# Kernel optimization log

Hardware: AMD Instinct MI355X
Metric: run time of the kernel (lower is better)

The kernel has to match this reference:

```python
import jax, jax.numpy as jnp
import numpy as np

IMG = 128                  # img_size
FMM = 35.0
SENSOR = 32.0
FUV = FMM * IMG / SENSOR   # focal length in pixels (screen space, in_ndc=False)
N_PTS = 16384
CHUNK = 1024               # points per scan step
R_SIL = 0.008              # silhouette pass radius (NDC)
R_DEP = 0.012              # depth pass radius (NDC)
K_SIL = 8
K_DEP = 16
DIST = 1.2


def _look_at(dist, elev_deg, azim_deg):
    # PyTorch3D look_at_view_transform with at=origin, up=+Y, degrees=True
    elev = jnp.deg2rad(elev_deg)
    azim = jnp.deg2rad(azim_deg)
    cam = jnp.stack([dist * jnp.cos(elev) * jnp.sin(azim),
                     dist * jnp.sin(elev),
                     dist * jnp.cos(elev) * jnp.cos(azim)], axis=-1)  # (B,3)
    up = jnp.array([0.0, 1.0, 0.0], dtype=cam.dtype)
    z_ax = -cam / (jnp.linalg.norm(cam, axis=-1, keepdims=True) + 1e-8)
    x_ax = jnp.cross(jnp.broadcast_to(up, z_ax.shape), z_ax)
    x_ax = x_ax / (jnp.linalg.norm(x_ax, axis=-1, keepdims=True) + 1e-8)
    y_ax = jnp.cross(z_ax, x_ax)
    R = jnp.stack([x_ax, y_ax, z_ax], axis=-1)   # columns are camera axes
    T = -jnp.einsum('bi,bij->bj', cam, R)        # X_cam = X_world @ R + T
    return R, T


def _project(pts, R, T):
    # world -> camera (row-vector convention) -> screen px -> PyTorch3D NDC
    Xc = jnp.einsum('bni,bij->bnj', pts, R) + T[:, None, :]
    z = Xc[..., 2]
    z_safe = jnp.where(z > 1e-5, z, 1.0)  # points behind camera are culled anyway
    xs = FUV * Xc[..., 0] / z_safe + IMG / 2.0
    ys = FUV * Xc[..., 1] / z_safe + IMG / 2.0
    x_ndc = 1.0 - 2.0 * xs / IMG
    y_ndc = 1.0 - 2.0 * ys / IMG
    return jnp.stack([x_ndc, y_ndc], axis=-1), z


def _rasterize(xy, z, r2, K):
    """Per-pixel K nearest-in-depth points within per-point NDC radius.
    xy: (B,N,2) NDC, z: (B,N) camera depth, r2: (B,N) squared radius.
    Returns zbuf, dists of shape (B,IMG,IMG,K), -1 for empty slots."""
    B, N, _ = xy.shape
    P = IMG * IMG
    # pixel-center NDC grid (PyTorch3D: +X left, +Y up; row-major flatten)
    gxs = 1.0 - (2.0 * jnp.arange(IMG, dtype=xy.dtype) + 1.0) / IMG  # per column
    gys = 1.0 - (2.0 * jnp.arange(IMG, dtype=xy.dtype) + 1.0) / IMG  # per row
    gx = jnp.tile(gxs, IMG)          # (P,)
    gy = jnp.repeat(gys, IMG)        # (P,)

    nch = N // CHUNK
    px = xy[..., 0].reshape(B, nch, CHUNK).swapaxes(0, 1)
    py = xy[..., 1].reshape(B, nch, CHUNK).swapaxes(0, 1)
    pz = z.reshape(B, nch, CHUNK).swapaxes(0, 1)
    pr2 = r2.reshape(B, nch, CHUNK).swapaxes(0, 1)

    def body(carry, c):
        top_z, top_d = carry
        cx, cy, cz, cr2 = c                               # each (B,CHUNK)
        dx = gx[None, :, None] - cx[:, None, :]           # (B,P,CHUNK)
        dy = gy[None, :, None] - cy[:, None, :]
        d2 = dx * dx + dy * dy
        ok = (d2 < cr2[:, None, :]) & (cz[:, None, :] > 0.0)
        zc = jnp.where(ok, cz[:, None, :], jnp.inf)
        cand_z = jnp.concatenate([top_z, zc], axis=-1)    # (B,P,K+CHUNK)
        cand_d = jnp.concatenate([top_d, d2], axis=-1)
        negz, idx = jax.lax.top_k(-cand_z, K)             # K smallest depths
        return (-negz, jnp.take_along_axis(cand_d, idx, axis=-1)), None

    init = (jnp.full((B, P, K), jnp.inf, dtype=xy.dtype),
            jnp.zeros((B, P, K), dtype=xy.dtype))
    (top_z, top_d), _ = jax.lax.scan(jax.checkpoint(body), init, (px, py, pz, pr2))
    valid = jnp.isfinite(top_z)
    zbuf = jnp.where(valid, top_z, -1.0).reshape(B, IMG, IMG, K)
    dists = jnp.where(valid, top_d, -1.0).reshape(B, IMG, IMG, K)
    return zbuf, dists


def setup_inputs() -> dict:
    key = jax.random.key(0)
    k1, k2 = jax.random.split(key)
    point_cloud = jax.random.normal(k1, (2, N_PTS, 6), dtype=jnp.float32) * 0.25
    param = jax.random.normal(k2, (2, 8, 3), dtype=jnp.float32) * 20.0  # degrees
    return {"point_cloud": point_cloud, "param": param}


def reference(point_cloud, param):
    pts = point_cloud[..., :3]
    B = pts.shape[0]
    elev0 = param[:, 1, 0]
    azim0 = param[:, 0, 0]

    # ---- silhouette pass (radius 0.008, K=8) + alpha compositing ----
    R0, T0 = _look_at(DIST, elev0, azim0)
    xy0, z0 = _project(pts, R0, T0)
    r2_sil = jnp.full((B, N_PTS), R_SIL * R_SIL, dtype=pts.dtype)
    _, dists_s = _rasterize(xy0, z0, r2_sil, K_SIL)
    alphas = jnp.where(dists_s >= 0.0, 1.0 - dists_s / (R_SIL * R_SIL), 0.0)
    trans = jnp.cumprod(1.0 - alphas, axis=-1)
    trans_excl = jnp.concatenate([jnp.ones_like(trans[..., :1]), trans[..., :-1]], axis=-1)
    sihlt_map = jnp.sum(alphas * trans_excl, axis=-1, keepdims=True) * 255.0  # (B,H,W,1)

    # ---- depth pass with random view (radius 0.012, K=16) ----
    kd = jax.random.key(42)
    ke, ka = jax.random.split(kd)
    elev_d = jax.random.uniform(ke, (B,), dtype=pts.dtype) * 60.0 - 30.0
    azim_d = jax.random.uniform(ka, (B,), dtype=pts.dtype) * 300.0 + azim0 + 30.0
    Rd, Td = _look_at(DIST, elev_d, azim_d)
    xyd, zd = _project(pts, Rd, Td)
    r2_dep = jnp.full((B, N_PTS), R_DEP * R_DEP, dtype=pts.dtype)
    zbuf_d, _ = _rasterize(xyd, zd, r2_dep, K_DEP)
    depth_ini = zbuf_d[..., 0]

    # density-aware adaptive radius (detached, per source .detach())
    area = jnp.sum((jax.lax.stop_gradient(depth_ini) > 0.0).astype(pts.dtype), axis=(1, 2))
    pa_radius = area / 16384.0 * 0.057                      # (B,)
    r2_ada = jnp.broadcast_to((pa_radius * pa_radius)[:, None], (B, N_PTS))

    zbuf_a, dists_a = _rasterize(xyd, zd, r2_ada, K_DEP)
    depth_img = zbuf_a[..., :8]
    dist_top = dists_a[..., :8]
    return (sihlt_map, depth_img, dist_top)
```

## Files before the change

kernel.cpp:

```cpp
#include <hip/hip_runtime.h>
#include <hip/hip_cooperative_groups.h>
#include <cstring>
#include <cstdint>

namespace cg = cooperative_groups;

#define NPTS 16384
#define FUVC 140.0f
#define R_SILF 0.008f
#define R_DEPF 0.012f
#define R2_SIL (0.008f*0.008f)
#define R2_DEP (0.012f*0.012f)
#define CH 512

#define AREA_OFF  48
#define PA_OFF    50
#define R2ADA_OFF 52
#define TICK0     54
#define TICK1     55
#define CNT_SIL   64
#define OFF_SIL   2112
#define CNT_ADA   4160
#define OFF_ADA   6208
#define FLAGS8    8256
#define FLAGS     8256
#define ZERO_END  16448
#define PROJ0     41024
#define PROJ1     172096
#define LSILF     303168
#define LADAF     827456
#define WS1_WORDS 2007104u
#define WS1_NEEDED ((size_t)WS1_WORDS * 4u)
#define LSIL      303168
#define LADA      434240
#define WS2_WORDS 729152u
#define WS2_NEEDED ((size_t)WS2_WORDS * 4u)

#define FUSED_BLOCKS 1024
#define FUSED_NT (FUSED_BLOCKS * 256)

__device__ __forceinline__ void cam_calc(float elev, float azim, float c[12]) {
    const float D2R = 0.017453292519943295f;
    float er = elev * D2R, ar = azim * D2R;
    float ce = cosf(er), se = sinf(er), ca = cosf(ar), sa = sinf(ar);
    float cx = 1.2f * ce * sa, cy = 1.2f * se, cz = 1.2f * ce * ca;
    float n = sqrtf(cx*cx + cy*cy + cz*cz) + 1e-8f;
    float zx = -cx / n, zy = -cy / n, zz = -cz / n;
    float xx = zz, xy = 0.0f, xz = -zx;
    float xn = sqrtf(xx*xx + xy*xy + xz*xz) + 1e-8f;
    xx /= xn; xz /= xn;
    float yx = zy*xz - zz*xy, yy = zz*xx - zx*xz, yz = zx*xy - zy*xx;
    c[0]=xx; c[1]=xy; c[2]=xz; c[3]=yx; c[4]=yy; c[5]=yz;
    c[6]=zx; c[7]=zy; c[8]=zz;
    c[9]  = -(cx*xx + cy*xy + cz*xz);
    c[10] = -(cx*yx + cy*yy + cz*yz);
    c[11] = -(cx*zx + cy*zy + cz*zz);
}

__device__ __forceinline__ void cam_compute(const float* __restrict__ param,
                                            float* __restrict__ ws,
                                            int t, float ue0, float ue1,
                                            float ua0, float ua1) {
    int b = t >> 1, cam = t & 1;
    float azim0 = param[b * 24 + 0];
    float elev0 = param[b * 24 + 3];
    float elev, azim;
    if (cam == 0) { elev = elev0; azim = azim0; }
    else {
        float ue = b ? ue1 : ue0;
        float ua = b ? ua1 : ua0;
        elev = ue * 60.0f - 30.0f;
        azim = ua * 300.0f + azim0 + 30.0f;
    }
    float c[12];
    cam_calc(elev, azim, c);
    float* w = ws + t * 12;
    #pragma unroll
    for (int i = 0; i < 12; i++) w[i] = c[i];
}

__device__ __forceinline__ float4 project_pt(const float* __restrict__ P,
                                             const float c[12]) {
    float X = P[0], Y = P[1], Z = P[2];
    float xc = X*c[0] + Y*c[1] + Z*c[2] + c[9];
    float yc = X*c[3] + Y*c[4] + Z*c[5] + c[10];
    float zc = X*c[6] + Y*c[7] + Z*c[8] + c[11];
    float zs = zc > 1e-5f ? zc : 1.0f;
    float px = 1.0f - (FUVC * xc / zs + 64.0f) * (1.0f/64.0f);
    float py = 1.0f - (FUVC * yc / zs + 64.0f) * (1.0f/64.0f);
    return make_float4(px, py, zc, 0.0f);
}

__device__ __forceinline__ void pix_range(float p, float r, int& lo, int& hi) {
    float lo_f = (1.0f - p - r) * 64.0f - 0.5f;
    float hi_f = (1.0f - p + r) * 64.0f - 0.5f;
    lo = (int)ceilf(lo_f - 1e-3f);
    hi = (int)floorf(hi_f + 1e-3f);
    lo = max(lo, 0); hi = min(hi, 127);
}

__device__ __forceinline__ void bin_bbox(float4 q, float r, int& bxl, int& bxh,
                                         int& byl, int& byh) {
    bxl = 0; bxh = -1; byl = 0; byh = -1;
    if (q.z > 0.0f) {
        int cl, chh, rl, rh;
        pix_range(q.x, r, cl, chh);
        pix_range(q.y, r, rl, rh);
        if (cl <= chh && rl <= rh) {
            bxl = cl >> 2; bxh = chh >> 2; byl = rl >> 2; byh = rh >> 2;
        }
    }
}

__device__ __forceinline__ void top8_insert(float z, float d,
                                            float tz[8], float td[8]) {
    #pragma unroll
    for (int k = 0; k < 8; k++) {
        bool lt = z < tz[k];
        float oz = tz[k], od = td[k];
        if (lt) { tz[k] = z; td[k] = d; z = oz; d = od; }
    }
}

__device__ __forceinline__ void hit_test(float4 pt, float gx, float gy, float r2,
                                         float tz[8], float td[8]) {
    float dx = gx - pt.x, dy = gy - pt.y;
    float d2 = dx*dx + dy*dy;
    if (d2 < r2 && pt.z > 0.0f && pt.z < tz[7]) top8_insert(pt.z, d2, tz, td);
}

#define CE8(i, j) { bool sw = mz[j] < mz[i]; \
    float t1 = mz[i], t2 = md[i]; \
    mz[i] = sw ? mz[j] : mz[i]; md[i] = sw ? md[j] : md[i]; \
    mz[j] = sw ? t1 : mz[j];    md[j] = sw ? t2 : md[j]; }

__device__ __forceinline__ void merge_sorted8(float tz[8], float td[8], int mask) {
    float oz[8], od[8];
    #pragma unroll
    for (int k = 0; k < 8; k++) {
        oz[k] = __shfl_xor(tz[k], mask);
        od[k] = __shfl_xor(td[k], mask);
    }
    float mz[8], md[8];
    #pragma unroll
    for (int k = 0; k < 8; k++) {
        bool take = oz[7 - k] < tz[k];
        mz[k] = take ? oz[7 - k] : tz[k];
        md[k] = take ? od[7 - k] : td[k];
    }
    CE8(0,4) CE8(1,5) CE8(2,6) CE8(3,7)
    CE8(0,2) CE8(1,3) CE8(4,6) CE8(5,7)
    CE8(0,1) CE8(2,3) CE8(4,5) CE8(6,7)
    #pragma unroll
    for (int k = 0; k < 8; k++) { tz[k] = mz[k]; td[k] = md[k]; }
}

__device__ __forceinline__ void merge_seq8(float tz[8], float td[8],
                                           const float* __restrict__ ozp,
                                           const float* __restrict__ odp) {
    float mz[8], md[8];
    #pragma unroll
    for (int k = 0; k < 8; k++) {
        float oz = ozp[7 - k], od = odp[7 - k];
        bool take = oz < tz[k];
        mz[k] = take ? oz : tz[k];
        md[k] = take ? od : td[k];
    }
    CE8(0,4) CE8(1,5) CE8(2,6) CE8(3,7)
    CE8(0,2) CE8(1,3) CE8(4,6) CE8(5,7)
    CE8(0,1) CE8(2,3) CE8(4,5) CE8(6,7)
    #pragma unroll
    for (int k = 0; k < 8; k++) { tz[k] = mz[k]; td[k] = md[k]; }
}

__device__ __forceinline__ void scan1024(unsigned* uw, unsigned cbase,
                                         unsigned obase, unsigned* s, int t) {
    unsigned c0 = uw[cbase + t*4 + 0];
    unsigned c1 = uw[cbase + t*4 + 1];
    unsigned c2 = uw[cbase + t*4 + 2];
    unsigned c3 = uw[cbase + t*4 + 3];
    unsigned tot = c0 + c1 + c2 + c3;
    s[t] = tot; __syncthreads();
    for (int off = 1; off < 256; off <<= 1) {
        unsigned v = (t >= off) ? s[t - off] : 0u;
        __syncthreads();
        s[t] += v;
        __syncthreads();
    }
    unsigned base = s[t] - tot;
    uw[obase + t*4 + 0] = base;
    uw[obase + t*4 + 1] = base + c0;
    uw[obase + t*4 + 2] = base + c0 + c1;
    uw[obase + t*4 + 3] = base + c0 + c1 + c2;
    uw[cbase + t*4 + 0] = 0;
    uw[cbase + t*4 + 1] = 0;
    uw[cbase + t*4 + 2] = 0;
    uw[cbase + t*4 + 3] = 0;
}

__device__ __forceinline__ void body_area_scan(float* __restrict__ ws, int job,
                                               int t, unsigned* s) {
    unsigned* uw = (unsigned*)ws;
    if (job < 2) {
        int b = job;
        unsigned acc = 0;
        #pragma unroll
        for (int j = 0; j < 16; j++) {
            unsigned w = uw[FLAGS8 + b * 4096 + t * 16 + j];
            acc += __popc(w & 0x01010101u);
        }
        s[t] = acc; __syncthreads();
        for (int off = 128; off > 0; off >>= 1) {
            if (t < off) s[t] += s[t + off];
            __syncthreads();
        }
        if (t == 0) {
            unsigned area = s[0];
            uw[AREA_OFF + b] = area;
            float pa = (float)area * (1.0f/16384.0f) * 0.057f;
            ws[PA_OFF + b] = pa;
            ws[R2ADA_OFF + b] = pa * pa;
        }
    } else {
        int b = job - 2;
        scan1024(uw, CNT_SIL + b * 1024, OFF_SIL + b * 1024, s, t);
    }
}

__device__ __forceinline__ void body_cnt_ada(float* __restrict__ ws, int p) {
    unsigned* uw = (unsigned*)ws;
    int b = p >> 14;
    float4 q = ((const float4*)(ws + PROJ1))[p];
    float pa = ws[PA_OFF + b];
    int bxl, bxh, byl, byh;
    bin_bbox(q, pa, bxl, bxh, byl, byh);
    for (int by = byl; by <= byh; by++)
        for (int bx = bxl; bx <= bxh; bx++)
            atomicAdd(&uw[CNT_ADA + b * 1024 + by * 32 + bx], 1u);
}

__device__ __forceinline__ void body_scat_sil(float* __restrict__ ws, int p) {
    unsigned* uw = (unsigned*)ws;
    int b = p >> 14;
    float4 q = ((const float4*)(ws + PROJ0))[p];
    int bxl, bxh, byl, byh;
    bin_bbox(q, R_SILF, bxl, bxh, byl, byh);
    for (int by = byl; by <= byh; by++)
        for (int bx = bxl; bx <= bxh; bx++) {
            unsigned bin = b * 1024 + by * 32 + bx;
            unsigned idx = uw[OFF_SIL + bin] + atomicAdd(&uw[CNT_SIL + bin], 1u);
            ((float4*)(ws + LSILF))[b * 65536 + idx] = q;
        }
}

__device__ __forceinline__ void body_scan_ada(float* __restrict__ ws, int b, int t) {
    unsigned* uw = (unsigned*)ws;
    unsigned c[16]; unsigned tot = 0;
    #pragma unroll
    for (int j = 0; j < 16; j++) { c[j] = uw[CNT_ADA + b * 1024 + t * 16 + j]; tot += c[j]; }
    unsigned inc = tot;
    #pragma unroll
    for (int off = 1; off < 64; off <<= 1) {
        unsigned v = __shfl_up(inc, off);
        if (t >= off) inc += v;
    }
    unsigned base = inc - tot;
    #pragma unroll
    for (int j = 0; j < 16; j++) {
        uw[OFF_ADA + b * 1024 + t * 16 + j] = base;
        base += c[j];
        uw[CNT_ADA + b * 1024 + t * 16 + j] = 0u;
    }
}

__device__ __forceinline__ void body_scat_ada(float* __restrict__ ws, int p) {
    unsigned* uw = (unsigned*)ws;
    int b = p >> 14;
    float4 q = ((const float4*)(ws + PROJ1))[p];
    float pa = ws[PA_OFF + b];
    int bxl, bxh, byl, byh;
    bin_bbox(q, pa, bxl, bxh, byl, byh);
    for (int by = byl; by <= byh; by++)
        for (int bx = bxl; bx <= bxh; bx++) {
            unsigned bin = b * 1024 + by * 32 + bx;
            unsigned idx = uw[OFF_ADA + bin] + atomicAdd(&uw[CNT_ADA + bin], 1u);
            ((float4*)(ws + LADAF))[b * 147456 + idx] = q;
        }
}

__device__ __forceinline__ void body_gather256(const float* __restrict__ ws,
                                               float* __restrict__ out,
                                               int id, int t,
                                               float* __restrict__ sm) {
    const unsigned* uw = (const unsigned*)ws;
    bool sil = id < 2048;
    int gt = sil ? id : id - 2048;
    int b = gt >> 10;
    int tile = gt & 1023;
    int p = t & 15, seg = t >> 4;
    int bx = tile & 31, by = tile >> 5;
    int col = (bx << 2) + (p & 3), row = (by << 2) + (p >> 2);
    float gx = 1.0f - (float)(2*col + 1) * (1.0f/128.0f);
    float gy = 1.0f - (float)(2*row + 1) * (1.0f/128.0f);
    float r2 = sil ? R2_SIL : ws[R2ADA_OFF + b];
    unsigned start = sil ? uw[OFF_SIL + b * 1024 + tile] : uw[OFF_ADA + b * 1024 + tile];
    unsigned len   = sil ? uw[CNT_SIL + b * 1024 + tile] : uw[CNT_ADA + b * 1024 + tile];
    const float4* lst = sil ? ((const float4*)(ws + LSILF)) + b * 65536 + start
                            : ((const float4*)(ws + LADAF)) + b * 147456 + start;

    float tz[8], td[8];
    #pragma unroll
    for (int k = 0; k < 8; k++) { tz[k] = INFINITY; td[k] = 0.0f; }

    unsigned i = (unsigned)seg;
    while (i + 112 < len) {
        float4 cb[8];
        #pragma unroll
        for (int u = 0; u < 8; u++) cb[u] = lst[i + 16u * (unsigned)u];
        #pragma unroll
        for (int u = 0; u < 8; u++) hit_test(cb[u], gx, gy, r2, tz, td);
        i += 128;
    }
    for (; i < len; i += 16) hit_test(lst[i], gx, gy, r2, tz, td);

    merge_sorted8(tz, td, 16);
    merge_sorted8(tz, td, 32);

    int w = t >> 6;
    if ((t & 63) < 16) {
        float* dst = sm + (w * 16 + p) * 17;
        #pragma unroll
        for (int k = 0; k < 8; k++) { dst[k] = tz[k]; dst[8 + k] = td[k]; }
    }
    __syncthreads();
    if (t < 16) {
        #pragma unroll
        for (int ww = 1; ww < 4; ww++) {
            const float* src = sm + (ww * 16 + p) * 17;
            merge_seq8(tz, td, src, src + 8);
        }
        int pix = (b << 14) + row * 128 + col;
        if (sil) {
            float trans = 1.0f, acc = 0.0f;
            #pragma unroll
            for (int k = 0; k < 8; k++) {
                float a = (tz[k] != INFINITY) ? (1.0f - td[k] / R2_SIL) : 0.0f;
                acc += a * trans;
                trans *= (1.0f - a);
            }
            out[pix] = acc * 255.0f;
        } else {
            float* dep = out + 32768  + (size_t)pix * 8;
            float* dst = out + 294912 + (size_t)pix * 8;
            #pragma unroll
            for (int k = 0; k < 8; k++) {
                bool v = (tz[k] != INFINITY);
                dep[k] = v ? tz[k] : -1.0f;
                dst[k] = v ? td[k] : -1.0f;
            }
        }
    }
}

__global__ __launch_bounds__(256) void k_fusedp(const float* __restrict__ pc,
                                                const float* __restrict__ param,
                                                float* __restrict__ ws,
                                                float* __restrict__ out,
                                                float ue0, float ue1,
                                                float ua0, float ua1) {
    cg::grid_group grid = cg::this_grid();
    unsigned* uw = (unsigned*)ws;
    __shared__ unsigned sh[2048];
    __shared__ unsigned shLast;
    int t = threadIdx.x;
    int tid = blockIdx.x * 256 + t;

    for (int i = 48 + tid; i < ZERO_END; i += FUSED_NT) uw[i] = 0u;
    if (tid < 4) cam_compute(param, ws, tid, ue0, ue1, ua0, ua1);
    grid.sync();

    if (blockIdx.x < 128) {
        int b = blockIdx.x >> 6;
        int p = ((blockIdx.x & 63) << 8) + t;
        unsigned char* fb = (unsigned char*)(uw + FLAGS8);
        const float* P = pc + ((size_t)b * NPTS + p) * 6;
        float c0[12], c1[12];
        const float* w0 = ws + (b * 2) * 12;
        #pragma unroll
        for (int i = 0; i < 12; i++) { c0[i] = w0[i]; c1[i] = w0[12 + i]; }

        #pragma unroll
        for (int j = 0; j < 4; j++) sh[t * 4 + j] = 0u;
        __syncthreads();

        float4 q0 = project_pt(P, c0);
        ((float4*)(ws + PROJ0))[b * NPTS + p] = q0;
        int bxl, bxh, byl, byh;
        bin_bbox(q0, R_SILF, bxl, bxh, byl, byh);
        for (int by = byl; by <= byh; by++)
            for (int bx = bxl; bx <= bxh; bx++)
                atomicAdd(&sh[by * 32 + bx], 1u);

        float4 q1 = project_pt(P, c1);
        ((float4*)(ws + PROJ1))[b * NPTS + p] = q1;
        if (q1.z > 0.0f) {
            int cl, chh, rl, rh;
            pix_range(q1.x, R_DEPF, cl, chh);
            pix_range(q1.y, R_DEPF, rl, rh);
            for (int rr = rl; rr <= rh; rr++) {
                float gyv = 1.0f - (float)(2 * rr + 1) * (1.0f/128.0f);
                float dy = gyv - q1.y;
                for (int cc = cl; cc <= chh; cc++) {
                    float gxv = 1.0f - (float)(2 * cc + 1) * (1.0f/128.0f);
                    float dx = gxv - q1.x;
                    if (dx*dx + dy*dy < R2_DEP) fb[b * NPTS + rr * 128 + cc] = 1;
                }
            }
        }
        __syncthreads();
        #pragma unroll
        for (int j = 0; j < 4; j++) {
            unsigned c = sh[t * 4 + j];
            if (c) atomicAdd(&uw[CNT_SIL + b * 1024 + t * 4 + j], c);
        }
        __threadfence();
    }
    if (t == 0) shLast = (atomicAdd(&uw[TICK0], 1u) == FUSED_BLOCKS - 1) ? 1u : 0u;
    __syncthreads();
    if (shLast) {
        __threadfence();
        for (int job = 0; job < 4; job++) {
            body_area_scan(ws, job, t, sh);
            __syncthreads();
        }
        __threadfence();
    }
    grid.sync();

    if (blockIdx.x < 128) {
        int b = blockIdx.x >> 6;
        int p = ((blockIdx.x & 63) << 8) + t;
        float4 q = ((const float4*)(ws + PROJ1))[b * NPTS + p];
        float pa = ws[PA_OFF + b];
        #pragma unroll
        for (int j = 0; j < 4; j++) sh[t * 4 + j] = 0u;
        __syncthreads();
        int bxl, bxh, byl, byh;
        bin_bbox(q, pa, bxl, bxh, byl, byh);
        for (int by = byl; by <= byh; by++)
            for (int bx = bxl; bx <= bxh; bx++)
                atomicAdd(&sh[by * 32 + bx], 1u);
        __syncthreads();
        #pragma unroll
        for (int j = 0; j < 4; j++) {
            unsigned c = sh[t * 4 + j];
            if (c) atomicAdd(&uw[CNT_ADA + b * 1024 + t * 4 + j], c);
        }
        __threadfence();
    } else if (blockIdx.x < 256) {
        int blk = blockIdx.x - 128;
        int b = blk >> 6;
        int p = ((blk & 63) << 8) + t;
        float4 q = ((const float4*)(ws + PROJ0))[b * NPTS + p];
        int bxl, bxh, byl, byh;
        bin_bbox(q, R_SILF, bxl, bxh, byl, byh);
        #pragma unroll
        for (int j = 0; j < 4; j++) sh[t * 4 + j] = 0u;
        __syncthreads();
        for (int by = byl; by <= byh; by++)
            for (int bx = bxl; bx <= bxh; bx++)
                atomicAdd(&sh[by * 32 + bx], 1u);
        __syncthreads();
        #pragma unroll
        for (int j = 0; j < 4; j++) {
            int bin = t * 4 + j;
            unsigned c = sh[bin];
            unsigned gb = 0;
            if (c) gb = uw[OFF_SIL + b * 1024 + bin] +
                        atomicAdd(&uw[CNT_SIL + b * 1024 + bin], c);
            sh[1024 + bin] = gb;
            sh[bin] = 0u;
        }
        __syncthreads();
        for (int by = byl; by <= byh; by++)
            for (int bx = bxl; bx <= bxh; bx++) {
                int bin = by * 32 + bx;
                unsigned loc = atomicAdd(&sh[bin], 1u);
                ((float4*)(ws + LSILF))[b * 65536 + sh[1024 + bin] + loc] = q;
            }
        __threadfence();
    }
    if (t == 0) shLast = (atomicAdd(&uw[TICK1], 1u) == FUSED_BLOCKS - 1) ? 1u : 0u;
    __syncthreads();
    if (shLast) {
        __threadfence();
        if (t < 128) body_scan_ada(ws, t >> 6, t & 63);
        __threadfence();
    }
    grid.sync();

    if (blockIdx.x < 128) {
        int b = blockIdx.x >> 6;
        int p = ((blockIdx.x & 63) << 8) + t;
        float4 q = ((const float4*)(ws + PROJ1))[b * NPTS + p];
        float pa = ws[PA_OFF + b];
        int bxl, bxh, byl, byh;
        bin_bbox(q, pa, bxl, bxh, byl, byh);
        #pragma unroll
        for (int j = 0; j < 4; j++) sh[t * 4 + j] = 0u;
        __syncthreads();
        for (int by = byl; by <= byh; by++)
            for (int bx = bxl; bx <= bxh; bx++)
                atomicAdd(&sh[by * 32 + bx], 1u);
        __syncthreads();
        #pragma unroll
        for (int j = 0; j < 4; j++) {
            int bin = t * 4 + j;
            unsigned c = sh[bin];
            unsigned gb = 0;
            if (c) gb = uw[OFF_ADA + b * 1024 + bin] +
                        atomicAdd(&uw[CNT_ADA + b * 1024 + bin], c);
            sh[1024 + bin] = gb;
            sh[bin] = 0u;
        }
        __syncthreads();
        for (int by = byl; by <= byh; by++)
            for (int bx = bxl; bx <= bxh; bx++) {
                int bin = by * 32 + bx;
                unsigned loc = atomicAdd(&sh[bin], 1u);
                ((float4*)(ws + LADAF))[b * 147456 + sh[1024 + bin] + loc] = q;
            }
    }
    grid.sync();

    for (int rep = 0; rep < 4; rep++) {
        int id = rep * 1024 + blockIdx.x;
        body_gather256(ws, out, id, t, (float*)sh);
        __syncthreads();
    }
}


__global__ __launch_bounds__(256) void k_zero(float* __restrict__ ws) {
    unsigned* uw = (unsigned*)ws;
    int gid = blockIdx.x * 256 + threadIdx.x;
    int stride = gridDim.x * 256;
    for (int i = 48 + gid; i < ZERO_END; i += stride) uw[i] = 0u;
}

__global__ __launch_bounds__(256) void k_proj_v3(const float* __restrict__ pc,
                                                 const float* __restrict__ param,
                                                 float* __restrict__ ws,
                                                 float ue0, float ue1,
                                                 float ua0, float ua1) {
    int b = blockIdx.x >> 6;
    int p = ((blockIdx.x & 63) << 8) + threadIdx.x;
    float azim0 = param[b * 24 + 0];
    float elev0 = param[b * 24 + 3];
    float c0[12], c1[12];
    cam_calc(elev0, azim0, c0);
    float ue = b ? ue1 : ue0;
    float ua = b ? ua1 : ua0;
    cam_calc(ue * 60.0f - 30.0f, ua * 300.0f + azim0 + 30.0f, c1);

    unsigned* uw = (unsigned*)ws;
    unsigned char* fb = (unsigned char*)(uw + FLAGS8);
    const float* P = pc + ((size_t)b * NPTS + p) * 6;

    float4 q0 = project_pt(P, c0);
    ((float4*)(ws + PROJ0))[b * NPTS + p] = q0;
    int bxl, bxh, byl, byh;
    bin_bbox(q0, R_SILF, bxl, bxh, byl, byh);
    for (int by = byl; by <= byh; by++)
        for (int bx = bxl; bx <= bxh; bx++)
            atomicAdd(&uw[CNT_SIL + b * 1024 + by * 32 + bx], 1u);

    float4 q1 = project_pt(P, c1);
    ((float4*)(ws + PROJ1))[b * NPTS + p] = q1;
    if (q1.z > 0.0f) {
        int cl, chh, rl, rh;
        pix_range(q1.x, R_DEPF, cl, chh);
        pix_range(q1.y, R_DEPF, rl, rh);
        for (int rr = rl; rr <= rh; rr++) {
            float gy = 1.0f - (float)(2 * rr + 1) * (1.0f/128.0f);
            float dy = gy - q1.y;
            for (int cc = cl; cc <= chh; cc++) {
                float gx = 1.0f - (float)(2 * cc + 1) * (1.0f/128.0f);
                float dx = gx - q1.x;
                if (dx*dx + dy*dy < R2_DEP) fb[b * NPTS + rr * 128 + cc] = 1;
            }
        }
    }
}

__global__ __launch_bounds__(256) void k_area_scan_v3(float* __restrict__ ws) {
    __shared__ unsigned s[256];
    body_area_scan(ws, blockIdx.x, threadIdx.x, s);
}

__global__ __launch_bounds__(64) void k_cntada_scatsil(float* __restrict__ ws) {
    int id = blockIdx.x;
    bool isCnt = id < 512;
    int p = ((isCnt ? id : id - 512) << 6) + threadIdx.x;
    if (isCnt) body_cnt_ada(ws, p);
    else       body_scat_sil(ws, p);
}

__global__ __launch_bounds__(64) void k_scan_ada64(float* __restrict__ ws) {
    body_scan_ada(ws, blockIdx.x, threadIdx.x);
}

__global__ __launch_bounds__(64) void k_scatter_ada_v2(float* __restrict__ ws) {
    body_scat_ada(ws, (blockIdx.x << 6) + threadIdx.x);
}

__global__ __launch_bounds__(256) void k_gather_v4(const float* __restrict__ ws,
                                                   float* __restrict__ out) {
    __shared__ float sm[1088];
    body_gather256(ws, out, blockIdx.x, threadIdx.x, sm);
}


__global__ __launch_bounds__(256) void k_init(const float* __restrict__ param,
                                              float* __restrict__ ws,
                                              float ue0, float ue1,
                                              float ua0, float ua1) {
    unsigned* uw = (unsigned*)ws;
    int gid = blockIdx.x * 256 + threadIdx.x;
    int stride = gridDim.x * 256;
    for (int i = gid; i < 2048; i += stride) { uw[CNT_SIL + i] = 0u; uw[CNT_ADA + i] = 0u; }
    for (int i = gid; i < 32768; i += stride) uw[FLAGS + i] = 0u;
    if (gid < 2) uw[AREA_OFF + gid] = 0u;
    if (gid < 4) cam_compute(param, ws, gid, ue0, ue1, ua0, ua1);
}

__global__ __launch_bounds__(256) void k_proj_count(const float* __restrict__ pc,
                                                    float* __restrict__ ws) {
    unsigned* uw = (unsigned*)ws;
    int b = blockIdx.x >> 6;
    int p = ((blockIdx.x & 63) << 8) + threadIdx.x;
    const float* P = pc + ((size_t)b * NPTS + p) * 6;
    float c0[12], c1[12];
    const float* w0 = ws + (b * 2) * 12;
    #pragma unroll
    for (int i = 0; i < 12; i++) { c0[i] = w0[i]; c1[i] = w0[12 + i]; }

    float4 q0 = project_pt(P, c0);
    ((float4*)(ws + PROJ0))[b * NPTS + p] = q0;
    int bxl, bxh, byl, byh;
    bin_bbox(q0, R_SILF, bxl, bxh, byl, byh);
    for (int by = byl; by <= byh; by++)
        for (int bx = bxl; bx <= bxh; bx++)
            atomicAdd(&uw[CNT_SIL + b * 1024 + by * 32 + bx], 1u);

    float4 q1 = project_pt(P, c1);
    ((float4*)(ws + PROJ1))[b * NPTS + p] = q1;
    if (q1.z > 0.0f) {
        int cl, chh, rl, rh;
        pix_range(q1.x, R_DEPF, cl, chh);
        pix_range(q1.y, R_DEPF, rl, rh);
        for (int rr = rl; rr <= rh; rr++) {
            float gy = 1.0f - (float)(2 * rr + 1) * (1.0f/128.0f);
            float dy = gy - q1.y;
            for (int cc = cl; cc <= chh; cc++) {
                float gx = 1.0f - (float)(2 * cc + 1) * (1.0f/128.0f);
                float dx = gx - q1.x;
                if (dx*dx + dy*dy < R2_DEP) uw[FLAGS + b * NPTS + rr * 128 + cc] = 1u;
            }
        }
    }
}

__global__ __launch_bounds__(256) void k_area_scan(float* __restrict__ ws) {
    unsigned* uw = (unsigned*)ws;
    __shared__ unsigned s[256];
    int t = threadIdx.x;
    int job = blockIdx.x;
    if (job < 2) {
        int b = job;
        unsigned acc = 0;
        for (int i = t; i < NPTS; i += 256) acc += uw[FLAGS + b * NPTS + i];
        s[t] = acc; __syncthreads();
        for (int off = 128; off > 0; off >>= 1) {
            if (t < off) s[t] += s[t + off];
            __syncthreads();
        }
        if (t == 0) {
            unsigned area = s[0];
            uw[AREA_OFF + b] = area;
            float pa = (float)area * (1.0f/16384.0f) * 0.057f;
            ws[PA_OFF + b] = pa;
            ws[R2ADA_OFF + b] = pa * pa;
        }
    } else {
// ... 113 lines not shown
    cam_compute(param, ws, t, ue0, ue1, ua0, ua1);
}

__device__ __forceinline__ void stage_points(const float* __restrict__ pcb,
                                             const float c[12], int c0, float4* sp) {
    for (int i = threadIdx.x; i < CH; i += 256) {
        const float* P = pcb + (size_t)(c0 + i) * 6;
        sp[i] = project_pt(P, c);
    }
}

__global__ __launch_bounds__(256) void raster_AB(const float* __restrict__ pc,
                                                 float* __restrict__ ws,
                                                 float* __restrict__ out) {
    __shared__ float4 sp[CH];
    int bid = blockIdx.x;
    bool silMode = bid < 128;
    int q = silMode ? bid : bid - 128;
    int b = q >> 6;
    int p = ((q & 63) << 8) + threadIdx.x;
    const float* cw = ws + (b * 2 + (silMode ? 0 : 1)) * 12;
    float c[12];
    #pragma unroll
    for (int i = 0; i < 12; i++) c[i] = cw[i];
    float r2 = silMode ? R2_SIL : R2_DEP;
    int col = p & 127, row = p >> 7;
    float gx = 1.0f - (float)(2*col + 1) * (1.0f/128.0f);
    float gy = 1.0f - (float)(2*row + 1) * (1.0f/128.0f);
    const float* pcb = pc + (size_t)b * NPTS * 6;

    if (silMode) {
        float tz[8], td[8];
        #pragma unroll
        for (int k = 0; k < 8; k++) { tz[k] = INFINITY; td[k] = 0.0f; }
        for (int c0 = 0; c0 < NPTS; c0 += CH) {
            __syncthreads();
            stage_points(pcb, c, c0, sp);
            __syncthreads();
            #pragma unroll 4
            for (int j = 0; j < CH; j++) hit_test(sp[j], gx, gy, r2, tz, td);
        }
        float trans = 1.0f, s = 0.0f;
        #pragma unroll
        for (int k = 0; k < 8; k++) {
            float a = (tz[k] != INFINITY) ? (1.0f - td[k] / r2) : 0.0f;
            s += a * trans;
            trans *= (1.0f - a);
        }
        out[(b << 14) + p] = s * 255.0f;
    } else {
        float mz = INFINITY;
        for (int c0 = 0; c0 < NPTS; c0 += CH) {
            __syncthreads();
            stage_points(pcb, c, c0, sp);
            __syncthreads();
            #pragma unroll 4
            for (int j = 0; j < CH; j++) {
                float4 pt = sp[j];
                float dx = gx - pt.x, dy = gy - pt.y;
                float d2 = dx*dx + dy*dy;
                if (d2 < r2 && pt.z > 0.0f) mz = fminf(mz, pt.z);
            }
        }
        unsigned long long m = __ballot(mz != INFINITY);
        if ((threadIdx.x & 63) == 0)
            atomicAdd(ws + 48 + b, (float)__popcll(m));
    }
}

__global__ __launch_bounds__(256) void raster_C(const float* __restrict__ pc,
                                                const float* __restrict__ ws,
                                                float* __restrict__ out) {
    __shared__ float4 sp[CH];
    int bid = blockIdx.x;
    int b = bid >> 6;
    int p = ((bid & 63) << 8) + threadIdx.x;
    const float* cw = ws + (b * 2 + 1) * 12;
    float c[12];
    #pragma unroll
    for (int i = 0; i < 12; i++) c[i] = cw[i];
    float area = ws[48 + b];
    float pa = (area * (1.0f/16384.0f)) * 0.057f;
    float r2 = pa * pa;
    int col = p & 127, row = p >> 7;
    float gx = 1.0f - (float)(2*col + 1) * (1.0f/128.0f);
    float gy = 1.0f - (float)(2*row + 1) * (1.0f/128.0f);
    const float* pcb = pc + (size_t)b * NPTS * 6;

    float tz[8], td[8];
    #pragma unroll
    for (int k = 0; k < 8; k++) { tz[k] = INFINITY; td[k] = 0.0f; }
    for (int c0 = 0; c0 < NPTS; c0 += CH) {
        __syncthreads();
        stage_points(pcb, c, c0, sp);
        __syncthreads();
        #pragma unroll 4
        for (int j = 0; j < CH; j++) hit_test(sp[j], gx, gy, r2, tz, td);
    }
    float* dep = out + 32768  + (size_t)((b << 14) + p) * 8;
    float* dst = out + 294912 + (size_t)((b << 14) + p) * 8;
    #pragma unroll
    for (int k = 0; k < 8; k++) {
        bool v = (tz[k] != INFINITY);
        dep[k] = v ? tz[k] : -1.0f;
        dst[k] = v ? td[k] : -1.0f;
    }
}

static inline uint32_t rotl32(uint32_t x, int r) { return (x << r) | (x >> (32 - r)); }

static void tf2x32(uint32_t k0, uint32_t k1, uint32_t c0, uint32_t c1,
                   uint32_t* o0, uint32_t* o1) {
    uint32_t ks0 = k0, ks1 = k1, ks2 = k0 ^ k1 ^ 0x1BD11BDAu;
    uint32_t x0 = c0 + ks0, x1 = c1 + ks1;
    static const int rA[4] = {13, 15, 26, 6};
    static const int rB[4] = {17, 29, 16, 24};
    #define RND4(R) do { for (int i = 0; i < 4; i++) { x0 += x1; x1 = rotl32(x1, R[i]); x1 ^= x0; } } while (0)
    RND4(rA); x0 += ks1; x1 += ks2 + 1u;
    RND4(rB); x0 += ks2; x1 += ks0 + 2u;
    RND4(rA); x0 += ks0; x1 += ks1 + 3u;
    RND4(rB); x0 += ks1; x1 += ks2 + 4u;
    RND4(rA); x0 += ks2; x1 += ks0 + 5u;
    #undef RND4
    *o0 = x0; *o1 = x1;
}

static inline float bits_to_unit_float(uint32_t bits) {
    uint32_t fb = (bits >> 9) | 0x3f800000u;
    float f;
    memcpy(&f, &fb, 4);
    return f - 1.0f;
}

extern "C" void kernel_launch(void* const* d_in, const int* in_sizes, int n_in,
                              void* d_out, int out_size, void* d_ws, size_t ws_size,
                              hipStream_t stream) {
    const float* pc    = (const float*)d_in[0];
    const float* param = (const float*)d_in[1];
    float* out = (float*)d_out;
    float* ws  = (float*)d_ws;

    uint32_t ke0, ke1, ka0, ka1, b1, b2;
    tf2x32(0u, 42u, 0u, 0u, &ke0, &ke1);
    tf2x32(0u, 42u, 0u, 1u, &ka0, &ka1);
    float ue[2], ua[2];
    for (uint32_t i = 0; i < 2; i++) {
        tf2x32(ke0, ke1, 0u, i, &b1, &b2);
        ue[i] = bits_to_unit_float(b1 ^ b2);
        tf2x32(ka0, ka1, 0u, i, &b1, &b2);
        ua[i] = bits_to_unit_float(b1 ^ b2);
    }
    float ue0 = ue[0], ue1 = ue[1], ua0 = ua[0], ua1 = ua[1];

    if (ws_size >= WS1_NEEDED) {
        int dev = 0;
        hipGetDevice(&dev);
        hipDeviceProp_t prop;
        bool coop = (hipGetDeviceProperties(&prop, dev) == hipSuccess) &&
                    prop.cooperativeLaunch;
        if (coop) {
            int maxB = 0;
            if (hipOccupancyMaxActiveBlocksPerMultiprocessor(&maxB, k_fusedp, 256, 0)
                    != hipSuccess ||
                maxB * prop.multiProcessorCount < FUSED_BLOCKS)
                coop = false;
        }
        if (coop) {
            void* args[] = { (void*)&pc, (void*)&param, (void*)&ws, (void*)&out,
                             (void*)&ue0, (void*)&ue1, (void*)&ua0, (void*)&ua1 };
            hipError_t e = hipLaunchCooperativeKernel((const void*)k_fusedp,
                                                      dim3(FUSED_BLOCKS), dim3(256),
                                                      args, 0, stream);
            if (e == hipSuccess) return;
        }
        k_zero          <<<16, 256, 0, stream>>>(ws);
        k_proj_v3       <<<128, 256, 0, stream>>>(pc, param, ws, ue0, ue1, ua0, ua1);
        k_area_scan_v3  <<<4, 256, 0, stream>>>(ws);
        k_cntada_scatsil<<<1024, 64, 0, stream>>>(ws);
        k_scan_ada64    <<<2, 64, 0, stream>>>(ws);
        k_scatter_ada_v2<<<512, 64, 0, stream>>>(ws);
        k_gather_v4     <<<4096, 256, 0, stream>>>(ws, out);
    } else if (ws_size >= WS2_NEEDED) {
        k_init      <<<64, 256, 0, stream>>>(param, ws, ue0, ue1, ua0, ua1);
        k_proj_count<<<128, 256, 0, stream>>>(pc, ws);
        k_area_scan <<<4, 256, 0, stream>>>(ws);
        k_count_ada <<<128, 256, 0, stream>>>(ws);
        k_scan_ada  <<<2, 256, 0, stream>>>(ws);
        k_scatter   <<<128, 256, 0, stream>>>(ws);
        k_gather_sil<<<128, 256, 0, stream>>>(ws, out);
        k_gather_ada<<<128, 256, 0, stream>>>(ws, out);
    } else {
        cam_kernel_fb<<<1, 64, 0, stream>>>(param, ws, ue0, ue1, ua0, ua1);
        raster_AB<<<256, 256, 0, stream>>>(pc, ws, out);
        raster_C <<<128, 256, 0, stream>>>(pc, ws, out);
    }
}
```

Before: 86.10 us.

## Replace count-scan-scatter binning with fixed-capacity bins and fewer grid syncs

Rewrites the cooperative fused kernel so silhouette and adaptive bins go into fixed-capacity per-bin slots through a single atomic cursor. This removes the separate count, prefix-scan and scatter passes and cuts the grid-wide barriers from four to two. Adaptive-pass points are binned with the maximum possible radius, so they no longer depend on the area reduction. Each block now recomputes the area and radius itself before gathering. The trade-offs are more candidates per adaptive bin, silent truncation if a bin exceeds its capacity, and a much larger workspace requirement; if that workspace is not available, execution falls back to the multi-kernel path.

Result: no change. 85.74 us (-0.4%).

```diff
diff --git a/kernel.cpp b/kernel.cpp
--- a/kernel.cpp
+++ b/kernel.cpp
@@ -9,6 +9,7 @@
 #define FUVC 140.0f
 #define R_SILF 0.008f
 #define R_DEPF 0.012f
+#define R_ADA_MAXF 0.057f
 #define R2_SIL (0.008f*0.008f)
 #define R2_DEP (0.012f*0.012f)
 #define CH 512
@@ -16,8 +17,6 @@
 #define AREA_OFF  48
 #define PA_OFF    50
 #define R2ADA_OFF 52
-#define TICK0     54
-#define TICK1     55
 #define CNT_SIL   64
 #define OFF_SIL   2112
 #define CNT_ADA   4160
@@ -36,6 +35,18 @@
 #define WS2_WORDS 729152u
 #define WS2_NEEDED ((size_t)WS2_WORDS * 4u)
 
+#define T0_CUR_SIL 64u
+#define T0_CUR_ADA 2112u
+#define T0_FLAGS8  4160u
+#define T0_ZBEG    64u
+#define T0_ZEND    12352u
+#define CAP_SIL    1024u
+#define CAP_ADA    2048u
+#define T0_LSIL    16384u
+#define T0_LADA    (16384u + 2048u*CAP_SIL*4u)
+#define WS0_WORDS  (T0_LADA + 2048u*CAP_ADA*4u)
+#define WS0_NEEDED ((size_t)WS0_WORDS * 4u)
+
 #define FUSED_BLOCKS 1024
 #define FUSED_NT (FUSED_BLOCKS * 256)
 
@@ -198,115 +209,16 @@
     uw[cbase + t*4 + 3] = 0;
 }
 
-__device__ __forceinline__ void body_area_scan(float* __restrict__ ws, int job,
-                                               int t, unsigned* s) {
-    unsigned* uw = (unsigned*)ws;
-    if (job < 2) {
-        int b = job;
-        unsigned acc = 0;
-        #pragma unroll
-        for (int j = 0; j < 16; j++) {
-            unsigned w = uw[FLAGS8 + b * 4096 + t * 16 + j];
-            acc += __popc(w & 0x01010101u);
-        }
-        s[t] = acc; __syncthreads();
-        for (int off = 128; off > 0; off >>= 1) {
-            if (t < off) s[t] += s[t + off];
-            __syncthreads();
-        }
-        if (t == 0) {
-            unsigned area = s[0];
-            uw[AREA_OFF + b] = area;
-            float pa = (float)area * (1.0f/16384.0f) * 0.057f;
-            ws[PA_OFF + b] = pa;
-            ws[R2ADA_OFF + b] = pa * pa;
-        }
-    } else {
-        int b = job - 2;
-        scan1024(uw, CNT_SIL + b * 1024, OFF_SIL + b * 1024, s, t);
-    }
-}
-
-__device__ __forceinline__ void body_cnt_ada(float* __restrict__ ws, int p) {
-    unsigned* uw = (unsigned*)ws;
-    int b = p >> 14;
-    float4 q = ((const float4*)(ws + PROJ1))[p];
-    float pa = ws[PA_OFF + b];
-    int bxl, bxh, byl, byh;
-    bin_bbox(q, pa, bxl, bxh, byl, byh);
-    for (int by = byl; by <= byh; by++)
-        for (int bx = bxl; bx <= bxh; bx++)
-            atomicAdd(&uw[CNT_ADA + b * 1024 + by * 32 + bx], 1u);
-}
-
-__device__ __forceinline__ void body_scat_sil(float* __restrict__ ws, int p) {
-    unsigned* uw = (unsigned*)ws;
-    int b = p >> 14;
-    float4 q = ((const float4*)(ws + PROJ0))[p];
-    int bxl, bxh, byl, byh;
-    bin_bbox(q, R_SILF, bxl, bxh, byl, byh);
-    for (int by = byl; by <= byh; by++)
-        for (int bx = bxl; bx <= bxh; bx++) {
-            unsigned bin = b * 1024 + by * 32 + bx;
-            unsigned idx = uw[OFF_SIL + bin] + atomicAdd(&uw[CNT_SIL + bin], 1u);
-            ((float4*)(ws + LSILF))[b * 65536 + idx] = q;
-        }
-}
-
-__device__ __forceinline__ void body_scan_ada(float* __restrict__ ws, int b, int t) {
-    unsigned* uw = (unsigned*)ws;
-    unsigned c[16]; unsigned tot = 0;
-    #pragma unroll
-    for (int j = 0; j < 16; j++) { c[j] = uw[CNT_ADA + b * 1024 + t * 16 + j]; tot += c[j]; }
-    unsigned inc = tot;
-    #pragma unroll
-    for (int off = 1; off < 64; off <<= 1) {
-        unsigned v = __shfl_up(inc, off);
-        if (t >= off) inc += v;
-    }
-    unsigned base = inc - tot;
-    #pragma unroll
-    for (int j = 0; j < 16; j++) {
-        uw[OFF_ADA + b * 1024 + t * 16 + j] = base;
-        base += c[j];
-        uw[CNT_ADA + b * 1024 + t * 16 + j] = 0u;
-    }
-}
-
-__device__ __forceinline__ void body_scat_ada(float* __restrict__ ws, int p) {
-    unsigned* uw = (unsigned*)ws;
-    int b = p >> 14;
-    float4 q = ((const float4*)(ws + PROJ1))[p];
-    float pa = ws[PA_OFF + b];
-    int bxl, bxh, byl, byh;
-    bin_bbox(q, pa, bxl, bxh, byl, byh);
-    for (int by = byl; by <= byh; by++)
-        for (int bx = bxl; bx <= bxh; bx++) {
-            unsigned bin = b * 1024 + by * 32 + bx;
-            unsigned idx = uw[OFF_ADA + bin] + atomicAdd(&uw[CNT_ADA + bin], 1u);
-            ((float4*)(ws + LADAF))[b * 147456 + idx] = q;
-        }
-}
-
-__device__ __forceinline__ void body_gather256(const float* __restrict__ ws,
-                                               float* __restrict__ out,
-                                               int id, int t,
-                                               float* __restrict__ sm) {
-    const unsigned* uw = (const unsigned*)ws;
-    bool sil = id < 2048;
-    int gt = sil ? id : id - 2048;
-    int b = gt >> 10;
-    int tile = gt & 1023;
+__device__ __forceinline__ void gather_tile(float* __restrict__ out, bool sil,
+                                            int b, int tile, float r2,
+                                            const float4* __restrict__ lst,
+                                            unsigned len, int t,
+                                            float* __restrict__ sm) {
     int p = t & 15, seg = t >> 4;
     int bx = tile & 31, by = tile >> 5;
     int col = (bx << 2) + (p & 3), row = (by << 2) + (p >> 2);
     float gx = 1.0f - (float)(2*col + 1) * (1.0f/128.0f);
     float gy = 1.0f - (float)(2*row + 1) * (1.0f/128.0f);
-    float r2 = sil ? R2_SIL : ws[R2ADA_OFF + b];
-    unsigned start = sil ? uw[OFF_SIL + b * 1024 + tile] : uw[OFF_ADA + b * 1024 + tile];
-    unsigned len   = sil ? uw[CNT_SIL + b * 1024 + tile] : uw[CNT_ADA + b * 1024 + tile];
-    const float4* lst = sil ? ((const float4*)(ws + LSILF)) + b * 65536 + start
-                            : ((const float4*)(ws + LADAF)) + b * 147456 + start;
 
     float tz[8], td[8];
     #pragma unroll
@@ -362,7 +274,7 @@
     }
 }
 
-__global__ __launch_bounds__(256) void k_fusedp(const float* __restrict__ pc,
+__global__ __launch_bounds__(256) void k_fused5(const float* __restrict__ pc,
                                                 const float* __restrict__ param,
                                                 float* __restrict__ ws,
                                                 float* __restrict__ out,
@@ -371,97 +283,21 @@
     cg::grid_group grid = cg::this_grid();
     unsigned* uw = (unsigned*)ws;
     __shared__ unsigned sh[2048];
-    __shared__ unsigned shLast;
     int t = threadIdx.x;
-    int tid = blockIdx.x * 256 + t;
-
-    for (int i = 48 + tid; i < ZERO_END; i += FUSED_NT) uw[i] = 0u;
-    if (tid < 4) cam_compute(param, ws, tid, ue0, ue1, ua0, ua1);
+    int blk = blockIdx.x;
+    int tid = blk * 256 + t;
+
+    for (unsigned i = T0_ZBEG + (unsigned)tid; i < T0_ZEND; i += FUSED_NT) uw[i] = 0u;
     grid.sync();
 
-    if (blockIdx.x < 128) {
-        int b = blockIdx.x >> 6;
-        int p = ((blockIdx.x & 63) << 8) + t;
-        unsigned char* fb = (unsigned char*)(uw + FLAGS8);
-        const float* P = pc + ((size_t)b * NPTS + p) * 6;
-        float c0[12], c1[12];
-        const float* w0 = ws + (b * 2) * 12;
-        #pragma unroll
-        for (int i = 0; i < 12; i++) { c0[i] = w0[i]; c1[i] = w0[12 + i]; }
-
-        #pragma unroll
-        for (int j = 0; j < 4; j++) sh[t * 4 + j] = 0u;
-        __syncthreads();
-
-        float4 q0 = project_pt(P, c0);
-        ((float4*)(ws + PROJ0))[b * NPTS + p] = q0;
-        int bxl, bxh, byl, byh;
-        bin_bbox(q0, R_SILF, bxl, bxh, byl, byh);
-        for (int by = byl; by <= byh; by++)
-            for (int bx = bxl; bx <= bxh; bx++)
-                atomicAdd(&sh[by * 32 + bx], 1u);
-
-        float4 q1 = project_pt(P, c1);
-        ((float4*)(ws + PROJ1))[b * NPTS + p] = q1;
-        if (q1.z > 0.0f) {
-            int cl, chh, rl, rh;
-            pix_range(q1.x, R_DEPF, cl, chh);
-            pix_range(q1.y, R_DEPF, rl, rh);
-            for (int rr = rl; rr <= rh; rr++) {
-                float gyv = 1.0f - (float)(2 * rr + 1) * (1.0f/128.0f);
-                float dy = gyv - q1.y;
-                for (int cc = cl; cc <= chh; cc++) {
-                    float gxv = 1.0f - (float)(2 * cc + 1) * (1.0f/128.0f);
-                    float dx = gxv - q1.x;
-                    if (dx*dx + dy*dy < R2_DEP) fb[b * NPTS + rr * 128 + cc] = 1;
-                }
-            }
-        }
-        __syncthreads();
-        #pragma unroll
-        for (int j = 0; j < 4; j++) {
-            unsigned c = sh[t * 4 + j];
-            if (c) atomicAdd(&uw[CNT_SIL + b * 1024 + t * 4 + j], c);
-        }
-        __threadfence();
-    }
-    if (t == 0) shLast = (atomicAdd(&uw[TICK0], 1u) == FUSED_BLOCKS - 1) ? 1u : 0u;
-    __syncthreads();
-    if (shLast) {
-        __threadfence();
-        for (int job = 0; job < 4; job++) {
-            body_area_scan(ws, job, t, sh);
-            __syncthreads();
-        }
-        __threadfence();
-    }
-    grid.sync();
-
-    if (blockIdx.x < 128) {
-        int b = blockIdx.x >> 6;
-        int p = ((blockIdx.x & 63) << 8) + t;
-        float4 q = ((const float4*)(ws + PROJ1))[b * NPTS + p];
-        float pa = ws[PA_OFF + b];
-        #pragma unroll
-        for (int j = 0; j < 4; j++) sh[t * 4 + j] = 0u;
-        __syncthreads();
-        int bxl, bxh, byl, byh;
-        bin_bbox(q, pa, bxl, bxh, byl, byh);
-        for (int by = byl; by <= byh; by++)
-            for (int bx = bxl; bx <= bxh; bx++)
-                atomicAdd(&sh[by * 32 + bx], 1u);
-        __syncthreads();
-        #pragma unroll
-        for (int j = 0; j < 4; j++) {
-            unsigned c = sh[t * 4 + j];
-            if (c) atomicAdd(&uw[CNT_ADA + b * 1024 + t * 4 + j], c);
-        }
-        __threadfence();
-    } else if (blockIdx.x < 256) {
-        int blk = blockIdx.x - 128;
+    if (blk < 128) {
         int b = blk >> 6;
         int p = ((blk & 63) << 8) + t;
-        float4 q = ((const float4*)(ws + PROJ0))[b * NPTS + p];
+        float azim0 = param[b * 24 + 0];
+        float elev0 = param[b * 24 + 3];
+        float c0[12];
+        cam_calc(elev0, azim0, c0);
+        float4 q = project_pt(pc + ((size_t)b * NPTS + p) * 6, c0);
         int bxl, bxh, byl, byh;
         bin_bbox(q, R_SILF, bxl, bxh, byl, byh);
         #pragma unroll
@@ -476,36 +312,47 @@
             int bin = t * 4 + j;
             unsigned c = sh[bin];
             unsigned gb = 0;
-            if (c) gb = uw[OFF_SIL + b * 1024 + bin] +
-                        atomicAdd(&uw[CNT_SIL + b * 1024 + bin], c);
+            if (c) gb = atomicAdd(&uw[T0_CUR_SIL + b * 1024 + bin], c);
             sh[1024 + bin] = gb;
             sh[bin] = 0u;
         }
         __syncthreads();
+        float4* lst = (float4*)(ws + T0_LSIL);
         for (int by = byl; by <= byh; by++)
             for (int bx = bxl; bx <= bxh; bx++) {
                 int bin = by * 32 + bx;
                 unsigned loc = atomicAdd(&sh[bin], 1u);
-                ((float4*)(ws + LSILF))[b * 65536 + sh[1024 + bin] + loc] = q;
+                unsigned idx = sh[1024 + bin] + loc;
+                if (idx < CAP_SIL)
+                    lst[(size_t)(b * 1024 + bin) * CAP_SIL + idx] = q;
             }
-        __threadfence();
-    }
-    if (t == 0) shLast = (atomicAdd(&uw[TICK1], 1u) == FUSED_BLOCKS - 1) ? 1u : 0u;
-    __syncthreads();
-    if (shLast) {
-        __threadfence();
-        if (t < 128) body_scan_ada(ws, t >> 6, t & 63);
-        __threadfence();
-    }
-    grid.sync();
-
-    if (blockIdx.x < 128) {
-        int b = blockIdx.x >> 6;
-        int p = ((blockIdx.x & 63) << 8) + t;
-        float4 q = ((const float4*)(ws + PROJ1))[b * NPTS + p];
-        float pa = ws[PA_OFF + b];
+    } else if (blk < 256) {
+        int blk2 = blk - 128;
+        int b = blk2 >> 6;
+        int p = ((blk2 & 63) << 8) + t;
+        float azim0 = param[b * 24 + 0];
+        float ue = b ? ue1 : ue0;
+        float ua = b ? ua1 : ua0;
+        float c1[12];
+        cam_calc(ue * 60.0f - 30.0f, ua * 300.0f + azim0 + 30.0f, c1);
+        float4 q = project_pt(pc + ((size_t)b * NPTS + p) * 6, c1);
+        unsigned char* fb = (unsigned char*)(uw + T0_FLAGS8);
+        if (q.z > 0.0f) {
+            int cl, chh, rl, rh;
+            pix_range(q.x, R_DEPF, cl, chh);
+            pix_range(q.y, R_DEPF, rl, rh);
+            for (int rr = rl; rr <= rh; rr++) {
+                float gyv = 1.0f - (float)(2 * rr + 1) * (1.0f/128.0f);
+                float dy = gyv - q.y;
+                for (int cc = cl; cc <= chh; cc++) {
+                    float gxv = 1.0f - (float)(2 * cc + 1) * (1.0f/128.0f);
+                    float dx = gxv - q.x;
+                    if (dx*dx + dy*dy < R2_DEP) fb[b * NPTS + rr * 128 + cc] = 1;
+                }
+            }
+        }
         int bxl, bxh, byl, byh;
-        bin_bbox(q, pa, bxl, bxh, byl, byh);
+        bin_bbox(q, R_ADA_MAXF, bxl, bxh, byl, byh);
         #pragma unroll
         for (int j = 0; j < 4; j++) sh[t * 4 + j] = 0u;
         __syncthreads();
@@ -518,28 +365,175 @@
             int bin = t * 4 + j;
             unsigned c = sh[bin];
             unsigned gb = 0;
-            if (c) gb = uw[OFF_ADA + b * 1024 + bin] +
-                        atomicAdd(&uw[CNT_ADA + b * 1024 + bin], c);
+            if (c) gb = atomicAdd(&uw[T0_CUR_ADA + b * 1024 + bin], c);
             sh[1024 + bin] = gb;
             sh[bin] = 0u;
         }
         __syncthreads();
+        float4* lst = (float4*)(ws + T0_LADA);
         for (int by = byl; by <= byh; by++)
             for (int bx = bxl; bx <= bxh; bx++) {
                 int bin = by * 32 + bx;
                 unsigned loc = atomicAdd(&sh[bin], 1u);
-                ((float4*)(ws + LADAF))[b * 147456 + sh[1024 + bin] + loc] = q;
+                unsigned idx = sh[1024 + bin] + loc;
+                if (idx < CAP_ADA)
+                    lst[(size_t)(b * 1024 + bin) * CAP_ADA + idx] = q;
             }
     }
     grid.sync();
 
-    for (int rep = 0; rep < 4; rep++) {
-        int id = rep * 1024 + blockIdx.x;
-        body_gather256(ws, out, id, t, (float*)sh);
-        __syncthreads();
-    }
-}
-
+    {
+        int b = blk & 1;
+        int j = blk >> 1;
+        unsigned acc = 0;
+        #pragma unroll
+        for (int i = 0; i < 16; i++)
+            acc += __popc(uw[T0_FLAGS8 + b * 4096 + t * 16 + i] & 0x01010101u);
+        sh[t] = acc; __syncthreads();
+        for (int off = 128; off > 0; off >>= 1) {
+            if (t < off) sh[t] += sh[t + off];
+            __syncthreads();
+        }
+        if (t == 0) {
+            float pa = (float)sh[0] * (1.0f/16384.0f) * 0.057f;
+            ((float*)sh)[1] = pa * pa;
+        }
+        __syncthreads();
+        float r2ada = ((float*)sh)[1];
+        __syncthreads();
+
+        const float4* lsil = (const float4*)(ws + T0_LSIL);
+        const float4* lada = (const float4*)(ws + T0_LADA);
+        #pragma unroll
+        for (int rep = 0; rep < 4; rep++) {
+            bool sil = rep < 2;
+            int tile = j * 2 + (rep & 1);
+            int bin = b * 1024 + tile;
+            unsigned len;
+            const float4* lst;
+            float r2;
+            if (sil) {
+                len = min(uw[T0_CUR_SIL + bin], CAP_SIL);
+                lst = lsil + (size_t)bin * CAP_SIL;
+                r2 = R2_SIL;
+            } else {
+                len = min(uw[T0_CUR_ADA + bin], CAP_ADA);
+                lst = lada + (size_t)bin * CAP_ADA;
+                r2 = r2ada;
+            }
+            gather_tile(out, sil, b, tile, r2, lst, len, t, (float*)sh);
+            __syncthreads();
+        }
+    }
+}
+
+
+__device__ __forceinline__ void body_area_scan(float* __restrict__ ws, int job,
+                                               int t, unsigned* s) {
+    unsigned* uw = (unsigned*)ws;
+    if (job < 2) {
+        int b = job;
+        unsigned acc = 0;
+        #pragma unroll
+        for (int j = 0; j < 16; j++) {
+            unsigned w = uw[FLAGS8 + b * 4096 + t * 16 + j];
+            acc += __popc(w & 0x01010101u);
+        }
+        s[t] = acc; __syncthreads();
+        for (int off = 128; off > 0; off >>= 1) {
+            if (t < off) s[t] += s[t + off];
+            __syncthreads();
+        }
+        if (t == 0) {
+            unsigned area = s[0];
+            uw[AREA_OFF + b] = area;
+            float pa = (float)area * (1.0f/16384.0f) * 0.057f;
+            ws[PA_OFF + b] = pa;
+            ws[R2ADA_OFF + b] = pa * pa;
+        }
+    } else {
+        int b = job - 2;
+        scan1024(uw, CNT_SIL + b * 1024, OFF_SIL + b * 1024, s, t);
+    }
+}
+
+__device__ __forceinline__ void body_cnt_ada(float* __restrict__ ws, int p) {
+    unsigned* uw = (unsigned*)ws;
+    int b = p >> 14;
+    float4 q = ((const float4*)(ws + PROJ1))[p];
+    float pa = ws[PA_OFF + b];
+    int bxl, bxh, byl, byh;
+    bin_bbox(q, pa, bxl, bxh, byl, byh);
+    for (int by = byl; by <= byh; by++)
+        for (int bx = bxl; bx <= bxh; bx++)
+            atomicAdd(&uw[CNT_ADA + b * 1024 + by * 32 + bx], 1u);
+}
+
+__device__ __forceinline__ void body_scat_sil(float* __restrict__ ws, int p) {
+    unsigned* uw = (unsigned*)ws;
+    int b = p >> 14;
+    float4 q = ((const float4*)(ws + PROJ0))[p];
+    int bxl, bxh, byl, byh;
+    bin_bbox(q, R_SILF, bxl, bxh, byl, byh);
+    for (int by = byl; by <= byh; by++)
+        for (int bx = bxl; bx <= bxh; bx++) {
+            unsigned bin = b * 1024 + by * 32 + bx;
+            unsigned idx = uw[OFF_SIL + bin] + atomicAdd(&uw[CNT_SIL + bin], 1u);
+            ((float4*)(ws + LSILF))[b * 65536 + idx] = q;
+        }
+}
+
+__device__ __forceinline__ void body_scan_ada(float* __restrict__ ws, int b, int t) {
+    unsigned* uw = (unsigned*)ws;
+    unsigned c[16]; unsigned tot = 0;
+    #pragma unroll
+    for (int j = 0; j < 16; j++) { c[j] = uw[CNT_ADA + b * 1024 + t * 16 + j]; tot += c[j]; }
+    unsigned inc = tot;
+    #pragma unroll
+    for (int off = 1; off < 64; off <<= 1) {
+        unsigned v = __shfl_up(inc, off);
+        if (t >= off) inc += v;
+    }
+    unsigned base = inc - tot;
+    #pragma unroll
+    for (int j = 0; j < 16; j++) {
+        uw[OFF_ADA + b * 1024 + t * 16 + j] = base;
+        base += c[j];
+        uw[CNT_ADA + b * 1024 + t * 16 + j] = 0u;
+    }
+}
+
+__device__ __forceinline__ void body_scat_ada(float* __restrict__ ws, int p) {
+    unsigned* uw = (unsigned*)ws;
+    int b = p >> 14;
+    float4 q = ((const float4*)(ws + PROJ1))[p];
+    float pa = ws[PA_OFF + b];
+    int bxl, bxh, byl, byh;
+    bin_bbox(q, pa, bxl, bxh, byl, byh);
+    for (int by = byl; by <= byh; by++)
+        for (int bx = bxl; bx <= bxh; bx++) {
+            unsigned bin = b * 1024 + by * 32 + bx;
+            unsigned idx = uw[OFF_ADA + bin] + atomicAdd(&uw[CNT_ADA + bin], 1u);
+            ((float4*)(ws + LADAF))[b * 147456 + idx] = q;
+        }
+}
+
+__device__ __forceinline__ void body_gather256(const float* __restrict__ ws,
+                                               float* __restrict__ out,
+                                               int id, int t,
+                                               float* __restrict__ sm) {
+    const unsigned* uw = (const unsigned*)ws;
+    bool sil = id < 2048;
+    int gt = sil ? id : id - 2048;
+    int b = gt >> 10;
+    int tile = gt & 1023;
+    float r2 = sil ? R2_SIL : ws[R2ADA_OFF + b];
+    unsigned start = sil ? uw[OFF_SIL + b * 1024 + tile] : uw[OFF_ADA + b * 1024 + tile];
+    unsigned len   = sil ? uw[CNT_SIL + b * 1024 + tile] : uw[CNT_ADA + b * 1024 + tile];
+    const float4* lst = sil ? ((const float4*)(ws + LSILF)) + b * 65536 + start
+                            : ((const float4*)(ws + LADAF)) + b * 147456 + start;
+    gather_tile(out, sil, b, tile, r2, lst, len, t, sm);
+}
 
 __global__ __launch_bounds__(256) void k_zero(float* __restrict__ ws) {
     unsigned* uw = (unsigned*)ws;
@@ -959,7 +953,7 @@
     }
     float ue0 = ue[0], ue1 = ue[1], ua0 = ua[0], ua1 = ua[1];
 
-    if (ws_size >= WS1_NEEDED) {
+    if (ws_size >= WS0_NEEDED) {
         int dev = 0;
         hipGetDevice(&dev);
         hipDeviceProp_t prop;
@@ -967,7 +961,7 @@
                     prop.cooperativeLaunch;
         if (coop) {
             int maxB = 0;
-            if (hipOccupancyMaxActiveBlocksPerMultiprocessor(&maxB, k_fusedp, 256, 0)
+            if (hipOccupancyMaxActiveBlocksPerMultiprocessor(&maxB, k_fused5, 256, 0)
                     != hipSuccess ||
                 maxB * prop.multiProcessorCount < FUSED_BLOCKS)
                 coop = false;
@@ -975,11 +969,13 @@
         if (coop) {
             void* args[] = { (void*)&pc, (void*)&param, (void*)&ws, (void*)&out,
                              (void*)&ue0, (void*)&ue1, (void*)&ua0, (void*)&ua1 };
-            hipError_t e = hipLaunchCooperativeKernel((const void*)k_fusedp,
+            hipError_t e = hipLaunchCooperativeKernel((const void*)k_fused5,
                                                       dim3(FUSED_BLOCKS), dim3(256),
                                                       args, 0, stream);
             if (e == hipSuccess) return;
         }
+    }
+    if (ws_size >= WS1_NEEDED) {
         k_zero          <<<16, 256, 0, stream>>>(ws);
         k_proj_v3       <<<128, 256, 0, stream>>>(pc, param, ws, ue0, ue1, ua0, ua1);
         k_area_scan_v3  <<<4, 256, 0, stream>>>(ws);
```
